# Optimization experiments

Measured on AMD Instinct MI355X. Metric: run time of the kernel, lower is better.

The kernel has to match this reference:

```python
import jax, jax.numpy as jnp
import numpy as np

C_S = 768
C_Z = 128
D = 32            # c_hidden (hardcoded in module)
H = C_S // D      # 24 heads
EPS = 1e-5
INF = 1e9


def setup_inputs() -> dict:
    key = jax.random.key(0)
    ks = jax.random.split(key, 16)
    B, S = 2, 1024
    n = lambda k, shp, s=1.0: jax.random.normal(k, shp, dtype=jnp.float32) * s
    return {
        "bs": n(ks[0], (B, S, C_S)),
        "z": n(ks[1], (S, S, C_Z)),
        "t": n(ks[2], (B, C_S)),
        "beta": n(ks[3], (B, S, S), 0.1),
        "z_mask": jax.random.randint(ks[4], (S, S), 0, 2).astype(jnp.int32),
        "w_adaln": n(ks[5], (C_S, 3 * C_S), 0.02),
        "b_adaln": n(ks[6], (3 * C_S,), 0.1),
        "ln_z_w": jnp.ones((C_Z,), jnp.float32),
        "ln_z_b": jnp.zeros((C_Z,), jnp.float32),
        "w_q": n(ks[7], (C_S, C_S), 0.02),
        "w_k": n(ks[8], (C_S, C_S), 0.02),
        "w_v": n(ks[9], (C_S, C_S), 0.02),
        "w_z": n(ks[10], (C_Z, H), 0.02),
        "rms_q_w": jnp.ones((D,), jnp.float32),
        "rms_k_w": jnp.ones((D,), jnp.float32),
        "w_o": n(ks[11], (C_S, C_S), 0.02),
        "b_o": jnp.zeros((C_S,), jnp.float32),
    }


def _ln(x, eps=EPS):
    mu = jnp.mean(x, axis=-1, keepdims=True)
    var = jnp.mean((x - mu) ** 2, axis=-1, keepdims=True)
    return (x - mu) * jax.lax.rsqrt(var + eps)


def _rms(x, w, eps=EPS):
    return x * jax.lax.rsqrt(jnp.mean(x * x, axis=-1, keepdims=True) + eps) * w


def reference(bs, z, t, beta, z_mask, w_adaln, b_adaln, ln_z_w, ln_z_b,
              w_q, w_k, w_v, w_z, rms_q_w, rms_k_w, w_o, b_o):
    B, S, _ = bs.shape
    # AdaLayerNormZero: SiLU(t) -> Linear -> (shift, scale, gate)
    emb = jax.nn.silu(t) @ w_adaln + b_adaln                # [B, 3*C_S]
    shift, scale, gate = jnp.split(emb, 3, axis=-1)
    bs_norm = _ln(bs) * (1.0 + scale[:, None, :]) + shift[:, None, :]
    gate = gate[:, None, :]                                  # [B,1,C_S]
    # LayerNorm on pair rep
    z_norm = _ln(z) * ln_z_w + ln_z_b                        # [S,S,C_Z]
    # Q/K/V with QK-RMSNorm
    q = _rms((bs_norm @ w_q).reshape(B, S, H, D).transpose(0, 2, 1, 3), rms_q_w)
    k = _rms((bs_norm @ w_k).reshape(B, S, H, D).transpose(0, 2, 1, 3), rms_k_w)
    v = (bs_norm @ w_v).reshape(B, S, H, D).transpose(0, 2, 1, 3)
    # pair bias [1,H,S,S] + mask bias + beta
    bias = jnp.einsum('ijc,ch->hij', z_norm, w_z)[None]
    mask_bias = jnp.where(z_mask.astype(jnp.float32) > 0.5, 0.0, -INF)[None, None]
    bias = bias + mask_bias + beta[:, None, :, :]
    scores = jnp.einsum('bhqd,bhkd->bhqk', q, k) * (1.0 / np.sqrt(D)) + bias
    attn = jax.nn.softmax(scores, axis=-1)
    out = jnp.einsum('bhqk,bhkd->bhqd', attn, v).transpose(0, 2, 1, 3).reshape(B, S, C_S)
    return (out @ w_o + b_o) * gate
```

## Files before the change

### kernel.cpp

```cpp
#include <hip/hip_runtime.h>
#include <hip/hip_bf16.h>
#include <math.h>

#define SQ 1024
#define CS 768
#define CZ 128
#define DD 32
#define NH 24
#define EPSV 1e-5f

typedef __hip_bfloat16 bf16;
typedef _Float16 f16;
typedef _Float16 f16x8 __attribute__((ext_vector_type(8)));
typedef _Float16 f16x4 __attribute__((ext_vector_type(4)));
typedef float f32x4 __attribute__((ext_vector_type(4)));

__device__ __forceinline__ float b2f(bf16 x) { return __bfloat162float(x); }
__device__ __forceinline__ bf16 f2b(float x) { return __float2bfloat16(x); }

__global__ __launch_bounds__(256) void k_adaln(const float* t, const float* w,
                                               const float* bias, float* emb) {
    __shared__ float st[CS];
    int b = blockIdx.y;
    int o = blockIdx.x * 256 + threadIdx.x;
    for (int c = threadIdx.x; c < CS; c += 256) {
        float x = t[b * CS + c];
        st[c] = x / (1.0f + __expf(-x));
    }
    __syncthreads();
    float acc = bias[o];
    for (int c = 0; c < CS; ++c)
        acc += st[c] * w[(size_t)c * (3 * CS) + o];
    emb[(size_t)b * 3 * CS + o] = acc;
}

__global__ __launch_bounds__(256) void k_bsnorm(const float* bs, const float* emb,
                                                f16* bsn) {
    int row = blockIdx.x;
    int b = row >> 10;
    const float* x = bs + (size_t)row * CS;
    float v[3], s1 = 0.f, s2 = 0.f;
    #pragma unroll
    for (int i = 0; i < 3; i++) {
        float f = x[threadIdx.x + i * 256];
        v[i] = f; s1 += f; s2 += f * f;
    }
    __shared__ float red[8];
    for (int off = 32; off; off >>= 1) { s1 += __shfl_down(s1, off); s2 += __shfl_down(s2, off); }
    int wid = threadIdx.x >> 6;
    if ((threadIdx.x & 63) == 0) { red[wid] = s1; red[wid + 4] = s2; }
    __syncthreads();
    s1 = red[0] + red[1] + red[2] + red[3];
    s2 = red[4] + red[5] + red[6] + red[7];
    float mu = s1 * (1.0f / CS);
    float var = s2 * (1.0f / CS) - mu * mu;
    float rs = rsqrtf(var + EPSV);
    const float* sh = emb + (size_t)b * 3 * CS;
    f16* o = bsn + (size_t)row * CS;
    #pragma unroll
    for (int i = 0; i < 3; i++) {
        int c = threadIdx.x + i * 256;
        o[c] = (f16)((v[i] - mu) * rs * (1.0f + sh[CS + c]) + sh[c]);
    }
}

__global__ __launch_bounds__(256) void k_wt(const float* wq, const float* wk,
                                            const float* wv, const float* wo,
                                            f16* wt) {
    int z = blockIdx.z;
    const float* W = (z == 0) ? wq : (z == 1) ? wk : (z == 2) ? wv : wo;
    f16* WT = wt + (size_t)z * CS * CS;
    __shared__ float ts[64][68];
    int t = threadIdx.x;
    int k0 = blockIdx.x * 64, n0 = blockIdx.y * 64;
    #pragma unroll
    for (int i = 0; i < 4; i++) {
        int kr = (t >> 4) + i * 16, nc = (t & 15) * 4;
        float4 v4 = *(const float4*)&W[(size_t)(k0 + kr) * CS + n0 + nc];
        ts[kr][nc] = v4.x; ts[kr][nc + 1] = v4.y;
        ts[kr][nc + 2] = v4.z; ts[kr][nc + 3] = v4.w;
    }
    __syncthreads();
    #pragma unroll
    for (int i = 0; i < 4; i++) {
        int nr = (t >> 4) + i * 16, kc = (t & 15) * 4;
        f16x4 h4;
        h4[0] = (f16)ts[kc][nr]; h4[1] = (f16)ts[kc + 1][nr];
        h4[2] = (f16)ts[kc + 2][nr]; h4[3] = (f16)ts[kc + 3][nr];
        *(f16x4*)&WT[(size_t)(n0 + nr) * CS + k0 + kc] = h4;
    }
}

#define GP 40
template<int MODE>
__global__ __launch_bounds__(256) void k_gemm16(const f16* A, const f16* WT,
                                                float* out, const float* rwq,
                                                const float* rwk, const float* b_o,
                                                const float* emb) {
    __shared__ f16 As[128 * GP];
    __shared__ f16 Ws[64 * GP];
    int t = threadIdx.x;
    int m0 = blockIdx.x * 128, n0 = blockIdx.y * 64;
    int z = blockIdx.z;
    const f16* Ab = A + (size_t)m0 * CS;
    const f16* Wb = WT + (size_t)z * CS * CS + (size_t)n0 * CS;
    if (MODE == 0) out += (size_t)z * ((size_t)2 * SQ * CS);
    int w = t >> 6, l = t & 63;
    int lg = l >> 4, ll = l & 15;
    int wr = w >> 1, wc = w & 1;
    int sr = t >> 2, sk = (t & 3) * 8;
    f32x4 acc[4][2] = {};
    for (int k0 = 0; k0 < CS; k0 += 32) {
        #pragma unroll
        for (int it = 0; it < 2; it++) {
            int r = sr + it * 64;
            *(f16x8*)&As[r * GP + sk] = *(const f16x8*)&Ab[(size_t)r * CS + k0 + sk];
        }
        *(f16x8*)&Ws[sr * GP + sk] = *(const f16x8*)&Wb[(size_t)sr * CS + k0 + sk];
        __syncthreads();
        f16x8 af[4], bf[2];
        #pragma unroll
        for (int mi = 0; mi < 4; mi++)
            af[mi] = *(const f16x8*)&As[(wr * 64 + mi * 16 + ll) * GP + lg * 8];
        #pragma unroll
        for (int ni = 0; ni < 2; ni++)
            bf[ni] = *(const f16x8*)&Ws[(wc * 32 + ni * 16 + ll) * GP + lg * 8];
        #pragma unroll
        for (int mi = 0; mi < 4; mi++)
            #pragma unroll
            for (int ni = 0; ni < 2; ni++)
                acc[mi][ni] = __builtin_amdgcn_mfma_f32_16x16x32_f16(
                    af[mi], bf[ni], acc[mi][ni], 0, 0, 0);
        __syncthreads();
    }
    int c0 = n0 + wc * 32;
    const float* rw = (z == 0) ? rwq : rwk;
    #pragma unroll
    for (int mi = 0; mi < 4; mi++) {
        #pragma unroll
        for (int rg = 0; rg < 4; rg++) {
            int r = m0 + wr * 64 + mi * 16 + lg * 4 + rg;
            int bb = r >> 10, s = r & 1023;
            float v0 = acc[mi][0][rg], v1 = acc[mi][1][rg];
            if (MODE == 0) {
                if (z < 2) {
                    float sq = v0 * v0 + v1 * v1;
                    sq += __shfl_xor(sq, 1); sq += __shfl_xor(sq, 2);
                    sq += __shfl_xor(sq, 4); sq += __shfl_xor(sq, 8);
                    float rs = rsqrtf(sq * (1.0f / DD) + EPSV);
                    v0 *= rs * rw[ll];
                    v1 *= rs * rw[16 + ll];
                }
                int h = c0 >> 5;
                float* op = out + (((size_t)bb * NH + h) * SQ + s) * DD;
                op[ll] = v0;
                op[16 + ll] = v1;
            } else {
                const float* gt = emb + (size_t)bb * 3 * CS + 2 * CS;
                out[(size_t)r * CS + c0 + ll] = (v0 + b_o[c0 + ll]) * gt[c0 + ll];
                out[(size_t)r * CS + c0 + 16 + ll] =
                    (v1 + b_o[c0 + 16 + ll]) * gt[c0 + 16 + ll];
            }
        }
    }
}

__global__ __launch_bounds__(64) void k_uv(const float* wz, const float* lnw,
                                           const float* lnb, float* uv) {
    int t = threadIdx.x;
    if (t < 2 * NH) {
        int h = t % NH;
        const float* s = (t < NH) ? lnw : lnb;
        float a = 0.f;
        for (int c = 0; c < CZ; ++c) a += s[c] * wz[c * NH + h];
        uv[t] = a;
    }
}

#define ZROWS 64
#define ZSTRIDE 132
__global__ __launch_bounds__(256) void k_zbias(const float* z, const int* zmask,
                                               const float* wz, const float* lnw,
                                               const float* lnb, const float* uv,
                                               bf16* zbias) {
    __shared__ float zt[ZROWS * ZSTRIDE];
    __shared__ bf16 ot[NH][ZROWS];
    int t = threadIdx.x;
    size_t base = (size_t)blockIdx.x * ZROWS;
    const float4* src = (const float4*)(z + base * CZ);
    #pragma unroll
    for (int it = 0; it < 8; it++) {
        int gi = t + it * 256;
        int row = gi >> 5, c4 = gi & 31;
        int cs = (c4 * 4) ^ ((row >> 3) << 2);
        *(float4*)&zt[row * ZSTRIDE + cs] = src[gi];
    }
    __syncthreads();
    int lane = t & 63;
    int qd = __builtin_amdgcn_readfirstlane(t >> 6);
    int sw = (lane >> 3) << 2;
    float acc[NH];
    #pragma unroll
    for (int h = 0; h < NH; h++) acc[h] = 0.f;
    float s1 = 0.f, s2 = 0.f;
    #pragma unroll
    for (int i = 0; i < 8; i++) {
        int c0 = qd * 32 + i * 4;
        float4 zv = *(const float4*)&zt[lane * ZSTRIDE + (c0 ^ sw)];
        float e[4] = {zv.x, zv.y, zv.z, zv.w};
        #pragma unroll
        for (int u = 0; u < 4; u++) {
            int c = c0 + u;
            float zval = e[u];
            s1 += zval;
            s2 = fmaf(zval, zval, s2);
            float tc = zval * lnw[c];
            #pragma unroll
            for (int h = 0; h < NH; h++)
                acc[h] = fmaf(tc, wz[c * NH + h], acc[h]);
        }
    }
    __syncthreads();
    {
        float* pp = zt + qd * (ZROWS * 27) + lane * 27;
        pp[0] = s1; pp[1] = s2;
        #pragma unroll
        for (int h = 0; h < NH; h++) pp[2 + h] = acc[h];
    }
    __syncthreads();
    int r = lane;
    int hb = qd * 6;
    float fs1 = 0.f, fs2 = 0.f;
    float fa[6] = {};
    #pragma unroll
    for (int q = 0; q < 4; q++) {
        const float* p = zt + q * (ZROWS * 27) + r * 27;
        fs1 += p[0]; fs2 += p[1];
        #pragma unroll
        for (int j = 0; j < 6; j++) fa[j] += p[2 + hb + j];
    }
    float mu = fs1 * (1.0f / CZ);
    float var = fs2 * (1.0f / CZ) - mu * mu;
    float rs = rsqrtf(var + EPSV);
    float mb = (zmask[base + r] > 0) ? 0.0f : -1.0e9f;
    #pragma unroll
    for (int j = 0; j < 6; j++) {
        int h = hb + j;
        float val = rs * fa[j] - mu * rs * uv[h] + uv[NH + h] + mb;
        ot[h][r] = f2b(val);
    }
    __syncthreads();
    size_t SS = (size_t)SQ * SQ;
    if (t < 192) {
        int h = t >> 3, l8 = t & 7;
        uint4 val = *(const uint4*)&ot[h][l8 * 8];
        *(uint4*)&zbias[(size_t)h * SS + base + l8 * 8] = val;
    }
}

#define PQK 40
#define PPV 72
__global__ __launch_bounds__(256) void k_attn(const float* q, const float* k,
                                              const float* v, const bf16* zbias,
                                              const float* beta, f16* attn_out) {
    int qt = blockIdx.x;
    int bh = blockIdx.y;
    int b = bh / NH, h = bh % NH;
    __shared__ f16 Qs[64 * PQK];
    __shared__ f16 Ks[64 * PQK];
    __shared__ f16 Vs[32 * PPV];
    __shared__ f16 Ps[64 * PPV];
    int t = threadIdx.x;
    int w = t >> 6, l = t & 63;
    int lg = l >> 4, ll = l & 15;
    const float scale = 0.17677669529663687f;
    size_t SS = (size_t)SQ * SQ;
    int srow = t >> 2, sc0 = (t & 3) * 8;

    {
        const float* qb = q + ((size_t)bh * SQ + qt * 64) * DD;
        float4 a0 = *(const float4*)&qb[srow * DD + sc0];
        float4 a1 = *(const float4*)&qb[srow * DD + sc0 + 4];
        f16x8 hv;
        hv[0] = (f16)(a0.x * scale); hv[1] = (f16)(a0.y * scale);
        hv[2] = (f16)(a0.z * scale); hv[3] = (f16)(a0.w * scale);
        hv[4] = (f16)(a1.x * scale); hv[5] = (f16)(a1.y * scale);
        hv[6] = (f16)(a1.z * scale); hv[7] = (f16)(a1.w * scale);
        *(f16x8*)&Qs[srow * PQK + sc0] = hv;
    }
    f32x4 accO0 = {0.f, 0.f, 0.f, 0.f}, accO1 = {0.f, 0.f, 0.f, 0.f};
    float m_reg[4], l_reg[4];
    #pragma unroll
    for (int r = 0; r < 4; r++) { m_reg[r] = -3.0e38f; l_reg[r] = 0.f; }

    float4 kr0, kr1, vr0, vr1;
    {
        const float* kb = k + ((size_t)bh * SQ) * DD;
        const float* vb = v + ((size_t)bh * SQ) * DD;
        kr0 = *(const float4*)&kb[srow * DD + sc0];
        kr1 = *(const float4*)&kb[srow * DD + sc0 + 4];
        vr0 = *(const float4*)&vb[srow * DD + sc0];
        vr1 = *(const float4*)&vb[srow * DD + sc0 + 4];
    }
    __syncthreads();
    {
        f16x8 hk;
        hk[0] = (f16)kr0.x; hk[1] = (f16)kr0.y; hk[2] = (f16)kr0.z; hk[3] = (f16)kr0.w;
        hk[4] = (f16)kr1.x; hk[5] = (f16)kr1.y; hk[6] = (f16)kr1.z; hk[7] = (f16)kr1.w;
        *(f16x8*)&Ks[srow * PQK + sc0] = hk;
        float vv[8] = {vr0.x, vr0.y, vr0.z, vr0.w, vr1.x, vr1.y, vr1.z, vr1.w};
        #pragma unroll
        for (int u = 0; u < 8; u++) Vs[(sc0 + u) * PPV + srow] = (f16)vv[u];
    }
    const unsigned short* zb = (const unsigned short*)(zbias + (size_t)h * SS);
    const float* bb = beta + (size_t)b * SS;
    int ibase = qt * 64 + w * 16 + lg * 4;

    for (int kt = 0; kt < 16; kt++) {
        __syncthreads();
        if (kt < 15) {
            const float* kb = k + ((size_t)bh * SQ + (kt + 1) * 64) * DD;
            const float* vb = v + ((size_t)bh * SQ + (kt + 1) * 64) * DD;
            kr0 = *(const float4*)&kb[srow * DD + sc0];
            kr1 = *(const float4*)&kb[srow * DD + sc0 + 4];
            vr0 = *(const float4*)&vb[srow * DD + sc0];
            vr1 = *(const float4*)&vb[srow * DD + sc0 + 4];
        }
        f32x4 acc[4];
        #pragma unroll
        for (int c = 0; c < 4; c++) {
            #pragma unroll
            for (int r = 0; r < 4; r++) {
                size_t off = (size_t)(ibase + r) * SQ + kt * 64 + c * 16 + ll;
                union { unsigned u; float f; } cv;
                cv.u = (unsigned)zb[off] << 16;
                acc[c][r] = cv.f + bb[off];
            }
        }
        f16x8 aQ = *(const f16x8*)&Qs[(w * 16 + ll) * PQK + lg * 8];
        #pragma unroll
        for (int c = 0; c < 4; c++) {
            f16x8 bK = *(const f16x8*)&Ks[(c * 16 + ll) * PQK + lg * 8];
            acc[c] = __builtin_amdgcn_mfma_f32_16x16x32_f16(aQ, bK, acc[c], 0, 0, 0);
        }
        float al[4];
        #pragma unroll
        for (int r = 0; r < 4; r++) {
            float mx = fmaxf(fmaxf(acc[0][r], acc[1][r]), fmaxf(acc[2][r], acc[3][r]));
            #pragma unroll
            for (int off = 1; off < 16; off <<= 1) mx = fmaxf(mx, __shfl_xor(mx, off, 64));
            float mn = fmaxf(m_reg[r], mx);
            al[r] = __expf(m_reg[r] - mn);
            float ps = 0.f;
            #pragma unroll
            for (int c = 0; c < 4; c++) {
                float p = __expf(acc[c][r] - mn);
                acc[c][r] = p;
                ps += p;
            }
            #pragma unroll
            for (int off = 1; off < 16; off <<= 1) ps += __shfl_xor(ps, off, 64);
            m_reg[r] = mn;
            l_reg[r] = l_reg[r] * al[r] + ps;
        }
        #pragma unroll
        for (int c = 0; c < 4; c++)
            #pragma unroll
            for (int r = 0; r < 4; r++)
                Ps[(w * 16 + lg * 4 + r) * PPV + c * 16 + ll] = (f16)acc[c][r];
        #pragma unroll
        for (int r = 0; r < 4; r++) { accO0[r] *= al[r]; accO1[r] *= al[r]; }
        __asm__ volatile("s_waitcnt lgkmcnt(0)" ::: "memory");
        #pragma unroll
        for (int jt = 0; jt < 2; jt++) {
            f16x8 aP = *(const f16x8*)&Ps[(w * 16 + ll) * PPV + jt * 32 + lg * 8];
            f16x8 bV0 = *(const f16x8*)&Vs[(ll) * PPV + jt * 32 + lg * 8];
            f16x8 bV1 = *(const f16x8*)&Vs[(16 + ll) * PPV + jt * 32 + lg * 8];
            accO0 = __builtin_amdgcn_mfma_f32_16x16x32_f16(aP, bV0, accO0, 0, 0, 0);
            accO1 = __builtin_amdgcn_mfma_f32_16x16x32_f16(aP, bV1, accO1, 0, 0, 0);
        }
        __syncthreads();
        if (kt < 15) {
            f16x8 hk;
            hk[0] = (f16)kr0.x; hk[1] = (f16)kr0.y; hk[2] = (f16)kr0.z; hk[3] = (f16)kr0.w;
            hk[4] = (f16)kr1.x; hk[5] = (f16)kr1.y; hk[6] = (f16)kr1.z; hk[7] = (f16)kr1.w;
            *(f16x8*)&Ks[srow * PQK + sc0] = hk;
            float vv[8] = {vr0.x, vr0.y, vr0.z, vr0.w, vr1.x, vr1.y, vr1.z, vr1.w};
            #pragma unroll
            for (int u = 0; u < 8; u++) Vs[(sc0 + u) * PPV + srow] = (f16)vv[u];
        }
    }
    #pragma unroll
    for (int r = 0; r < 4; r++) {
        float inv = 1.0f / l_reg[r];
        int row = qt * 64 + w * 16 + lg * 4 + r;
        f16* op = attn_out + ((size_t)b * SQ + row) * CS + h * DD;
        op[ll] = (f16)(accO0[r] * inv);
        op[16 + ll] = (f16)(accO1[r] * inv);
    }
}

extern "C" void kernel_launch(void* const* d_in, const int* in_sizes, int n_in,
                              void* d_out, int out_size, void* d_ws, size_t ws_size,
                              hipStream_t stream) {
    const float* bs      = (const float*)d_in[0];
    const float* z       = (const float*)d_in[1];
    const float* t       = (const float*)d_in[2];
    const float* beta    = (const float*)d_in[3];
    const int*   z_mask  = (const int*)d_in[4];
    const float* w_adaln = (const float*)d_in[5];
    const float* b_adaln = (const float*)d_in[6];
    const float* ln_z_w  = (const float*)d_in[7];
    const float* ln_z_b  = (const float*)d_in[8];
    const float* w_q     = (const float*)d_in[9];
    const float* w_k     = (const float*)d_in[10];
    const float* w_v     = (const float*)d_in[11];
    const float* w_z     = (const float*)d_in[12];
    const float* rms_q_w = (const float*)d_in[13];
    const float* rms_k_w = (const float*)d_in[14];
    const float* w_o     = (const float*)d_in[15];
    const float* b_o     = (const float*)d_in[16];
    float* out = (float*)d_out;

    char* ws = (char*)d_ws;
    const size_t SZ_QKV = (size_t)2 * SQ * CS * 4;
    float* emb   = (float*)(ws);
    f16*   bsn   = (f16*)(ws + 32768);
    float* qbuf  = (float*)(ws + 32768 + SZ_QKV);
    float* kbuf  = (float*)(ws + 32768 + 2 * SZ_QKV);
    float* vbuf  = (float*)(ws + 32768 + 3 * SZ_QKV);
    f16*   attn  = (f16*)(ws + 32768 + 4 * SZ_QKV);
    bf16*  zbias = (bf16*)(ws + 32768 + 5 * SZ_QKV);
    float* uv    = (float*)(ws + 32768 + 5 * SZ_QKV + 50331648);
    f16*   wt    = (f16*)(ws + 32768 + 5 * SZ_QKV + 50331648 + 4096);

    k_adaln<<<dim3(9, 2), 256, 0, stream>>>(t, w_adaln, b_adaln, emb);
    k_uv<<<1, 64, 0, stream>>>(w_z, ln_z_w, ln_z_b, uv);
    k_wt<<<dim3(12, 12, 4), 256, 0, stream>>>(w_q, w_k, w_v, w_o, wt);
    k_bsnorm<<<2048, 256, 0, stream>>>(bs, emb, bsn);
    k_gemm16<0><<<dim3(16, 12, 3), 256, 0, stream>>>(bsn, wt, qbuf, rms_q_w,
                                                     rms_k_w, nullptr, nullptr);
    k_zbias<<<16384, 256, 0, stream>>>(z, z_mask, w_z, ln_z_w, ln_z_b, uv, zbias);
    k_attn<<<dim3(16, 48), 256, 0, stream>>>(qbuf, kbuf, vbuf, zbias, beta, attn);
    k_gemm16<1><<<dim3(16, 12, 1), 256, 0, stream>>>(attn, wt + (size_t)3 * CS * CS,
                                                     out, nullptr, nullptr, b_o, emb);
}
```

Baseline: 920.6 us.

## Widen GEMM tiles to 128x128 and use lazy softmax rescaling in attention

The projection GEMMs now use 128x128 tiles with four N-fragments per wave, increasing operand reuse and halving the block count. The attention kernel skips max reduction and rescaling unless some lane's local max exceeds the running max by a threshold, and it defers the row-sum shuffle reduction to the end. This removes per-tile cross-lane shuffles and exp rescales. The trade-offs are fewer blocks for the small output GEMM and larger unnormalized exponentials held in f16.

After: 915.4 us. Within noise of the previous version (-0.6%).

```diff
diff --git a/kernel.cpp b/kernel.cpp
--- a/kernel.cpp
+++ b/kernel.cpp
@@ -98,9 +98,9 @@
                                                 const float* rwk, const float* b_o,
                                                 const float* emb) {
     __shared__ f16 As[128 * GP];
-    __shared__ f16 Ws[64 * GP];
+    __shared__ f16 Ws[128 * GP];
     int t = threadIdx.x;
-    int m0 = blockIdx.x * 128, n0 = blockIdx.y * 64;
+    int m0 = blockIdx.x * 128, n0 = blockIdx.y * 128;
     int z = blockIdx.z;
     const f16* Ab = A + (size_t)m0 * CS;
     const f16* Wb = WT + (size_t)z * CS * CS + (size_t)n0 * CS;
@@ -108,32 +108,32 @@
     int w = t >> 6, l = t & 63;
     int lg = l >> 4, ll = l & 15;
     int wr = w >> 1, wc = w & 1;
-    int sr = t >> 2, sk = (t & 3) * 8;
-    f32x4 acc[4][2] = {};
+    f32x4 acc[4][4] = {};
     for (int k0 = 0; k0 < CS; k0 += 32) {
         #pragma unroll
         for (int it = 0; it < 2; it++) {
-            int r = sr + it * 64;
-            *(f16x8*)&As[r * GP + sk] = *(const f16x8*)&Ab[(size_t)r * CS + k0 + sk];
-        }
-        *(f16x8*)&Ws[sr * GP + sk] = *(const f16x8*)&Wb[(size_t)sr * CS + k0 + sk];
+            int seg = t + it * 256;
+            int r = seg >> 2, cs8 = (seg & 3) * 8;
+            *(f16x8*)&As[r * GP + cs8] = *(const f16x8*)&Ab[(size_t)r * CS + k0 + cs8];
+            *(f16x8*)&Ws[r * GP + cs8] = *(const f16x8*)&Wb[(size_t)r * CS + k0 + cs8];
+        }
         __syncthreads();
-        f16x8 af[4], bf[2];
+        f16x8 af[4], bf[4];
         #pragma unroll
         for (int mi = 0; mi < 4; mi++)
             af[mi] = *(const f16x8*)&As[(wr * 64 + mi * 16 + ll) * GP + lg * 8];
         #pragma unroll
-        for (int ni = 0; ni < 2; ni++)
-            bf[ni] = *(const f16x8*)&Ws[(wc * 32 + ni * 16 + ll) * GP + lg * 8];
+        for (int ni = 0; ni < 4; ni++)
+            bf[ni] = *(const f16x8*)&Ws[(wc * 64 + ni * 16 + ll) * GP + lg * 8];
         #pragma unroll
         for (int mi = 0; mi < 4; mi++)
             #pragma unroll
-            for (int ni = 0; ni < 2; ni++)
+            for (int ni = 0; ni < 4; ni++)
                 acc[mi][ni] = __builtin_amdgcn_mfma_f32_16x16x32_f16(
                     af[mi], bf[ni], acc[mi][ni], 0, 0, 0);
         __syncthreads();
     }
-    int c0 = n0 + wc * 32;
+    int c0 = n0 + wc * 64;
     const float* rw = (z == 0) ? rwq : rwk;
     #pragma unroll
     for (int mi = 0; mi < 4; mi++) {
@@ -141,25 +141,30 @@
         for (int rg = 0; rg < 4; rg++) {
             int r = m0 + wr * 64 + mi * 16 + lg * 4 + rg;
             int bb = r >> 10, s = r & 1023;
-            float v0 = acc[mi][0][rg], v1 = acc[mi][1][rg];
             if (MODE == 0) {
-                if (z < 2) {
-                    float sq = v0 * v0 + v1 * v1;
-                    sq += __shfl_xor(sq, 1); sq += __shfl_xor(sq, 2);
-                    sq += __shfl_xor(sq, 4); sq += __shfl_xor(sq, 8);
-                    float rs = rsqrtf(sq * (1.0f / DD) + EPSV);
-                    v0 *= rs * rw[ll];
-                    v1 *= rs * rw[16 + ll];
+                #pragma unroll
+                for (int pr = 0; pr < 2; pr++) {
+                    float v0 = acc[mi][pr * 2][rg], v1 = acc[mi][pr * 2 + 1][rg];
+                    if (z < 2) {
+                        float sq = v0 * v0 + v1 * v1;
+                        sq += __shfl_xor(sq, 1); sq += __shfl_xor(sq, 2);
+                        sq += __shfl_xor(sq, 4); sq += __shfl_xor(sq, 8);
+                        float rsq = rsqrtf(sq * (1.0f / DD) + EPSV);
+                        v0 *= rsq * rw[ll];
+                        v1 *= rsq * rw[16 + ll];
+                    }
+                    int h = (c0 + pr * 32) >> 5;
+                    float* op = out + (((size_t)bb * NH + h) * SQ + s) * DD;
+                    op[ll] = v0;
+                    op[16 + ll] = v1;
                 }
-                int h = c0 >> 5;
-                float* op = out + (((size_t)bb * NH + h) * SQ + s) * DD;
-                op[ll] = v0;
-                op[16 + ll] = v1;
             } else {
                 const float* gt = emb + (size_t)bb * 3 * CS + 2 * CS;
-                out[(size_t)r * CS + c0 + ll] = (v0 + b_o[c0 + ll]) * gt[c0 + ll];
-                out[(size_t)r * CS + c0 + 16 + ll] =
-                    (v1 + b_o[c0 + 16 + ll]) * gt[c0 + 16 + ll];
+                #pragma unroll
+                for (int ni = 0; ni < 4; ni++) {
+                    int col = c0 + ni * 16 + ll;
+                    out[(size_t)r * CS + col] = (acc[mi][ni][rg] + b_o[col]) * gt[col];
+                }
             }
         }
     }
@@ -289,9 +294,9 @@
         *(f16x8*)&Qs[srow * PQK + sc0] = hv;
     }
     f32x4 accO0 = {0.f, 0.f, 0.f, 0.f}, accO1 = {0.f, 0.f, 0.f, 0.f};
-    float m_reg[4], l_reg[4];
-    #pragma unroll
-    for (int r = 0; r < 4; r++) { m_reg[r] = -3.0e38f; l_reg[r] = 0.f; }
+    float m_reg[4], l_part[4];
+    #pragma unroll
+    for (int r = 0; r < 4; r++) { m_reg[r] = -3.0e38f; l_part[r] = 0.f; }
 
     float4 kr0, kr1, vr0, vr1;
     {
@@ -343,33 +348,34 @@
             f16x8 bK = *(const f16x8*)&Ks[(c * 16 + ll) * PQK + lg * 8];
             acc[c] = __builtin_amdgcn_mfma_f32_16x16x32_f16(aQ, bK, acc[c], 0, 0, 0);
         }
-        float al[4];
         #pragma unroll
         for (int r = 0; r < 4; r++) {
-            float mx = fmaxf(fmaxf(acc[0][r], acc[1][r]), fmaxf(acc[2][r], acc[3][r]));
-            #pragma unroll
-            for (int off = 1; off < 16; off <<= 1) mx = fmaxf(mx, __shfl_xor(mx, off, 64));
-            float mn = fmaxf(m_reg[r], mx);
-            al[r] = __expf(m_reg[r] - mn);
+            float lm = fmaxf(fmaxf(acc[0][r], acc[1][r]), fmaxf(acc[2][r], acc[3][r]));
+            if (__any(lm > m_reg[r] + 8.0f)) {
+                float mx = lm;
+                #pragma unroll
+                for (int off = 1; off < 16; off <<= 1) mx = fmaxf(mx, __shfl_xor(mx, off, 64));
+                float mn = fmaxf(m_reg[r], mx);
+                float al = __expf(m_reg[r] - mn);
+                m_reg[r] = mn;
+                l_part[r] *= al;
+                accO0[r] *= al;
+                accO1[r] *= al;
+            }
             float ps = 0.f;
             #pragma unroll
             for (int c = 0; c < 4; c++) {
-                float p = __expf(acc[c][r] - mn);
+                float p = __expf(acc[c][r] - m_reg[r]);
                 acc[c][r] = p;
                 ps += p;
             }
-            #pragma unroll
-            for (int off = 1; off < 16; off <<= 1) ps += __shfl_xor(ps, off, 64);
-            m_reg[r] = mn;
-            l_reg[r] = l_reg[r] * al[r] + ps;
+            l_part[r] += ps;
         }
         #pragma unroll
         for (int c = 0; c < 4; c++)
             #pragma unroll
             for (int r = 0; r < 4; r++)
                 Ps[(w * 16 + lg * 4 + r) * PPV + c * 16 + ll] = (f16)acc[c][r];
-        #pragma unroll
-        for (int r = 0; r < 4; r++) { accO0[r] *= al[r]; accO1[r] *= al[r]; }
         __asm__ volatile("s_waitcnt lgkmcnt(0)" ::: "memory");
         #pragma unroll
         for (int jt = 0; jt < 2; jt++) {
@@ -392,7 +398,10 @@
     }
     #pragma unroll
     for (int r = 0; r < 4; r++) {
-        float inv = 1.0f / l_reg[r];
+        float lf = l_part[r];
+        lf += __shfl_xor(lf, 1, 64); lf += __shfl_xor(lf, 2, 64);
+        lf += __shfl_xor(lf, 4, 64); lf += __shfl_xor(lf, 8, 64);
+        float inv = 1.0f / lf;
         int row = qt * 64 + w * 16 + lg * 4 + r;
         f16* op = attn_out + ((size_t)b * SQ + row) * CS + h * DD;
         op[ll] = (f16)(accO0[r] * inv);
@@ -438,10 +447,10 @@
     k_uv<<<1, 64, 0, stream>>>(w_z, ln_z_w, ln_z_b, uv);
     k_wt<<<dim3(12, 12, 4), 256, 0, stream>>>(w_q, w_k, w_v, w_o, wt);
     k_bsnorm<<<2048, 256, 0, stream>>>(bs, emb, bsn);
-    k_gemm16<0><<<dim3(16, 12, 3), 256, 0, stream>>>(bsn, wt, qbuf, rms_q_w,
-                                                     rms_k_w, nullptr, nullptr);
+    k_gemm16<0><<<dim3(16, 6, 3), 256, 0, stream>>>(bsn, wt, qbuf, rms_q_w,
+                                                    rms_k_w, nullptr, nullptr);
     k_zbias<<<16384, 256, 0, stream>>>(z, z_mask, w_z, ln_z_w, ln_z_b, uv, zbias);
     k_attn<<<dim3(16, 48), 256, 0, stream>>>(qbuf, kbuf, vbuf, zbias, beta, attn);
-    k_gemm16<1><<<dim3(16, 12, 1), 256, 0, stream>>>(attn, wt + (size_t)3 * CS * CS,
-                                                     out, nullptr, nullptr, b_o, emb);
-}
+    k_gemm16<1><<<dim3(16, 6, 1), 256, 0, stream>>>(attn, wt + (size_t)3 * CS * CS,
+                                                    out, nullptr, nullptr, b_o, emb);
+}
```
